# Optimization experiments

Hardware: AMD Instinct MI355X
Metric: run time of the kernel (lower is better)

## Reference

```python
import jax, jax.numpy as jnp
import numpy as np

TEMPERATURE = 8.0  # sqrt(d_k=64)


def setup_inputs() -> dict:
    key = jax.random.key(0)
    kq, kk, kv, km = jax.random.split(key, 4)
    B, S, D = 64, 2048, 64
    q = jax.random.normal(kq, (B, S, D), dtype=jnp.float32)
    k = jax.random.normal(kk, (B, S, D), dtype=jnp.float32)
    v = jax.random.normal(kv, (B, S, D), dtype=jnp.float32)
    mask = jax.random.randint(km, (B, S, S), 0, 2).astype(bool)
    return {"q": q, "k": k, "v": v, "mask": mask}


def reference(q, k, v, mask):
    # attn = q @ k^T / temperature, masked positions -> -inf
    scores = jnp.einsum("bqd,bkd->bqk", q, k) / TEMPERATURE
    scores = jnp.where(mask, -jnp.inf, scores)
    attn = jax.nn.softmax(scores, axis=-1)
    # dropout is identity in eval mode (deterministic reference)
    output = jnp.einsum("bqk,bkd->bqd", attn, v)
    return (output, attn)
```

## Files before the change

### kernel.cpp

```cpp
#include <hip/hip_runtime.h>
#include <math.h>

#define B 64
#define S 2048
#define D 64
#define INV_TEMP 0.125f

__global__ __launch_bounds__(256) void attn_scores_kernel(
    const float* __restrict__ qp, const float* __restrict__ kp,
    const int* __restrict__ maskp, float* __restrict__ attnp)
{
    __shared__ float kt[64][68];

    const int b    = blockIdx.y;
    const int wave = threadIdx.x >> 6;
    const int lane = threadIdx.x & 63;
    const int row  = blockIdx.x * 4 + wave;

    const float4* qrow = (const float4*)(qp + ((size_t)b * S + row) * D);
    float4 q4[16];
#pragma unroll
    for (int i = 0; i < 16; ++i) q4[i] = qrow[i];

    const size_t arow_base = ((size_t)b * S + row) * S;
    const float* kbase = kp + (size_t)b * S * D;

    float e[32];
    float rowsum = 0.f;

#pragma unroll
    for (int t = 0; t < 32; ++t) {
        __syncthreads();
        {
            const float4* ksrc = (const float4*)(kbase + (size_t)t * 64 * D);
#pragma unroll
            for (int i = 0; i < 4; ++i) {
                int idx = threadIdx.x + 256 * i;
                int r  = idx >> 4;
                int c4 = idx & 15;
                *((float4*)&kt[r][c4 * 4]) = ksrc[idx];
            }
        }
        __syncthreads();

        float s = 0.f;
#pragma unroll
        for (int d4 = 0; d4 < 16; ++d4) {
            float4 kv = *((const float4*)&kt[lane][d4 * 4]);
            s += q4[d4].x * kv.x + q4[d4].y * kv.y + q4[d4].z * kv.z + q4[d4].w * kv.w;
        }
        int m = maskp[arow_base + (size_t)t * 64 + lane];
        float ev = m ? 0.f : __expf(s * INV_TEMP);
        e[t] = ev;
        rowsum += ev;
    }

    float sum = rowsum;
#pragma unroll
    for (int off = 32; off > 0; off >>= 1) sum += __shfl_xor(sum, off, 64);
    float inv = 1.0f / sum;

    float* arow = attnp + arow_base;
#pragma unroll
    for (int t = 0; t < 32; ++t) arow[(size_t)t * 64 + lane] = e[t] * inv;
}

__global__ __launch_bounds__(256) void attn_pv_kernel(
    const float* __restrict__ attnp, const float* __restrict__ vp,
    float* __restrict__ outp)
{
    __shared__ float at[16][64];
    __shared__ float red[4][16][64];

    const int b  = blockIdx.y;
    const int r0 = blockIdx.x * 16;
    const int t  = threadIdx.x;
    const int d  = t & 63;
    const int g  = t >> 6;

    const float* vbase = vp + (size_t)b * S * D;
    const float* abase = attnp + ((size_t)b * S + r0) * S;

    float acc[16];
#pragma unroll
    for (int r = 0; r < 16; ++r) acc[r] = 0.f;

    for (int kt = 0; kt < 32; ++kt) {
        __syncthreads();
#pragma unroll
        for (int i = 0; i < 4; ++i) {
            int idx = t + 256 * i;
            at[idx >> 6][idx & 63] =
                abase[(size_t)(idx >> 6) * S + (size_t)kt * 64 + (idx & 63)];
        }
        __syncthreads();

#pragma unroll
        for (int kk = 0; kk < 16; ++kk) {
            int kl = g * 16 + kk;
            float vv = vbase[(size_t)(kt * 64 + kl) * D + d];
#pragma unroll
            for (int r = 0; r < 16; ++r) acc[r] += at[r][kl] * vv;
        }
    }

#pragma unroll
    for (int r = 0; r < 16; ++r) red[g][r][d] = acc[r];
    __syncthreads();
#pragma unroll
    for (int i = 0; i < 4; ++i) {
        int idx = t + 256 * i;
        int r = idx >> 6, dd = idx & 63;
        float sum = red[0][r][dd] + red[1][r][dd] + red[2][r][dd] + red[3][r][dd];
        outp[((size_t)b * S + r0 + r) * D + dd] = sum;
    }
}

extern "C" void kernel_launch(void* const* d_in, const int* in_sizes, int n_in,
                              void* d_out, int out_size, void* d_ws, size_t ws_size,
                              hipStream_t stream) {
    const float* q = (const float*)d_in[0];
    const float* k = (const float*)d_in[1];
    const float* v = (const float*)d_in[2];
    const int* mask = (const int*)d_in[3];

    float* out  = (float*)d_out;
    float* attn = out + (size_t)B * S * D;

    attn_scores_kernel<<<dim3(S / 4, B), 256, 0, stream>>>(q, k, mask, attn);
    attn_pv_kernel<<<dim3(S / 16, B), 256, 0, stream>>>(attn, v, out);
}
```

Baseline: 4.157 ms.

## Fuse QK, softmax numerator and PV into one tiled kernel with deferred normalization

Replaces the scores kernel and the PV kernel with one fused kernel. Each block handles 64 query rows, computes 4x4 register-tiled QK^T from swizzled shared memory, applies the mask and exp, writes the unnormalized probabilities, and accumulates P·V on the fly with K/V prefetched into registers. Row sums are reduced at the end to normalize the output, and a separate light kernel rescales the attention matrix in place. This avoids re-reading the full attention matrix for PV, at the cost of an extra read-modify-write pass over it for normalization.

```diff
diff --git a/kernel.cpp b/kernel.cpp
--- a/kernel.cpp
+++ b/kernel.cpp
@@ -6,113 +6,200 @@
 #define D 64
 #define INV_TEMP 0.125f
 
-__global__ __launch_bounds__(256) void attn_scores_kernel(
+__global__ __launch_bounds__(256) void attn_fused_kernel(
     const float* __restrict__ qp, const float* __restrict__ kp,
-    const int* __restrict__ maskp, float* __restrict__ attnp)
+    const float* __restrict__ vp, const int* __restrict__ maskp,
+    float* __restrict__ attnp, float* __restrict__ outp)
 {
-    __shared__ float kt[64][68];
-
+    __shared__ float qs[64][64];
+    __shared__ float ks[64][64];
+    __shared__ float vs[64][64];
+    __shared__ float es[64][64];
+
+    const int bid = blockIdx.x;
+    const int swz = (bid & 7) * 256 + (bid >> 3);
+    const int b   = swz >> 5;
+    const int r0  = (swz & 31) * 64;
+
+    const int t    = threadIdx.x;
+    const int tr   = t >> 4;
+    const int tc   = t & 15;
+    const int rr   = tr * 4;
+    const int cc   = tc * 4;
+    const int qxor = (tr & 7) << 2;
+    const int kxor = (tc & 7) << 2;
+
+    const float* kbase = kp + (size_t)b * S * D;
+    const float* vbase = vp + (size_t)b * S * D;
+
+    {
+        const float4* qsrc = (const float4*)(qp + ((size_t)b * S + r0) * D);
+#pragma unroll
+        for (int i = 0; i < 4; ++i) {
+            int idx = t + 256 * i;
+            int r = idx >> 4;
+            int c = (idx & 15) * 4;
+            *(float4*)&qs[r][c ^ (((r >> 2) & 7) << 2)] = qsrc[idx];
+        }
+    }
+
+    float4 acc[4];
+#pragma unroll
+    for (int i = 0; i < 4; ++i) acc[i] = make_float4(0.f, 0.f, 0.f, 0.f);
+    float rs[4] = {0.f, 0.f, 0.f, 0.f};
+
+    float4 kreg[4], vreg[4];
+    {
+        const float4* ksrc = (const float4*)kbase;
+        const float4* vsrc = (const float4*)vbase;
+#pragma unroll
+        for (int i = 0; i < 4; ++i) {
+            kreg[i] = ksrc[t + 256 * i];
+            vreg[i] = vsrc[t + 256 * i];
+        }
+    }
+#pragma unroll
+    for (int i = 0; i < 4; ++i) {
+        int idx = t + 256 * i;
+        int r = idx >> 4;
+        int c = (idx & 15) * 4;
+        *(float4*)&ks[r][c ^ (((r >> 2) & 7) << 2)] = kreg[i];
+        *(float4*)&vs[r][c] = vreg[i];
+    }
+    __syncthreads();
+
+#pragma unroll 1
+    for (int kt = 0; kt < 32; ++kt) {
+        if (kt < 31) {
+            const float4* ksrc = (const float4*)(kbase + (size_t)(kt + 1) * 64 * D);
+            const float4* vsrc = (const float4*)(vbase + (size_t)(kt + 1) * 64 * D);
+#pragma unroll
+            for (int i = 0; i < 4; ++i) {
+                kreg[i] = ksrc[t + 256 * i];
+                vreg[i] = vsrc[t + 256 * i];
+            }
+        }
+        int4 m4[4];
+#pragma unroll
+        for (int i = 0; i < 4; ++i) {
+            m4[i] = *(const int4*)(maskp + ((size_t)b * S + r0 + rr + i) * S
+                                   + (size_t)kt * 64 + cc);
+        }
+
+        float sc[4][4];
+#pragma unroll
+        for (int i = 0; i < 4; ++i)
+#pragma unroll
+            for (int j = 0; j < 4; ++j) sc[i][j] = 0.f;
+
+#pragma unroll
+        for (int dstep = 0; dstep < 16; ++dstep) {
+            const int dc = dstep * 4;
+            float4 q4[4], k4[4];
+#pragma unroll
+            for (int i = 0; i < 4; ++i) q4[i] = *(const float4*)&qs[rr + i][dc ^ qxor];
+#pragma unroll
+            for (int j = 0; j < 4; ++j) k4[j] = *(const float4*)&ks[cc + j][dc ^ kxor];
+#pragma unroll
+            for (int i = 0; i < 4; ++i)
+#pragma unroll
+                for (int j = 0; j < 4; ++j)
+                    sc[i][j] += q4[i].x * k4[j].x + q4[i].y * k4[j].y
+                              + q4[i].z * k4[j].z + q4[i].w * k4[j].w;
+        }
+
+        const size_t abase = ((size_t)b * S + r0 + rr) * S + (size_t)kt * 64 + cc;
+#pragma unroll
+        for (int i = 0; i < 4; ++i) {
+            float4 e4;
+            e4.x = m4[i].x ? 0.f : __expf(sc[i][0] * INV_TEMP);
+            e4.y = m4[i].y ? 0.f : __expf(sc[i][1] * INV_TEMP);
+            e4.z = m4[i].z ? 0.f : __expf(sc[i][2] * INV_TEMP);
+            e4.w = m4[i].w ? 0.f : __expf(sc[i][3] * INV_TEMP);
+            rs[i] += (e4.x + e4.y) + (e4.z + e4.w);
+            *(float4*)&es[rr + i][cc ^ qxor] = e4;
+            *(float4*)(attnp + abase + (size_t)i * S) = e4;
+        }
+        __syncthreads();
+
+#pragma unroll
+        for (int kk = 0; kk < 64; kk += 4) {
+            float4 e4[4], v4[4];
+#pragma unroll
+            for (int i = 0; i < 4; ++i) e4[i] = *(const float4*)&es[rr + i][kk ^ qxor];
+#pragma unroll
+            for (int u = 0; u < 4; ++u) v4[u] = *(const float4*)&vs[kk + u][cc];
+#pragma unroll
+            for (int i = 0; i < 4; ++i) {
+                acc[i].x += e4[i].x * v4[0].x + e4[i].y * v4[1].x
+                          + e4[i].z * v4[2].x + e4[i].w * v4[3].x;
+                acc[i].y += e4[i].x * v4[0].y + e4[i].y * v4[1].y
+                          + e4[i].z * v4[2].y + e4[i].w * v4[3].y;
+                acc[i].z += e4[i].x * v4[0].z + e4[i].y * v4[1].z
+                          + e4[i].z * v4[2].z + e4[i].w * v4[3].z;
+                acc[i].w += e4[i].x * v4[0].w + e4[i].y * v4[1].w
+                          + e4[i].z * v4[2].w + e4[i].w * v4[3].w;
+            }
+        }
+        __syncthreads();
+
+        if (kt < 31) {
+#pragma unroll
+            for (int i = 0; i < 4; ++i) {
+                int idx = t + 256 * i;
+                int r = idx >> 4;
+                int c = (idx & 15) * 4;
+                *(float4*)&ks[r][c ^ (((r >> 2) & 7) << 2)] = kreg[i];
+                *(float4*)&vs[r][c] = vreg[i];
+            }
+            __syncthreads();
+        }
+    }
+
+#pragma unroll
+    for (int i = 0; i < 4; ++i) {
+        float s = rs[i];
+        s += __shfl_xor(s, 1, 64);
+        s += __shfl_xor(s, 2, 64);
+        s += __shfl_xor(s, 4, 64);
+        s += __shfl_xor(s, 8, 64);
+        const float inv = 1.f / s;
+        float4 o;
+        o.x = acc[i].x * inv;
+        o.y = acc[i].y * inv;
+        o.z = acc[i].z * inv;
+        o.w = acc[i].w * inv;
+        *(float4*)(outp + ((size_t)b * S + r0 + rr + i) * D + cc) = o;
+    }
+}
+
+__global__ __launch_bounds__(256) void attn_norm_kernel(float* __restrict__ attnp)
+{
     const int b    = blockIdx.y;
     const int wave = threadIdx.x >> 6;
     const int lane = threadIdx.x & 63;
     const int row  = blockIdx.x * 4 + wave;
 
-    const float4* qrow = (const float4*)(qp + ((size_t)b * S + row) * D);
-    float4 q4[16];
-#pragma unroll
-    for (int i = 0; i < 16; ++i) q4[i] = qrow[i];
-
-    const size_t arow_base = ((size_t)b * S + row) * S;
-    const float* kbase = kp + (size_t)b * S * D;
-
-    float e[32];
-    float rowsum = 0.f;
-
-#pragma unroll
-    for (int t = 0; t < 32; ++t) {
-        __syncthreads();
-        {
-            const float4* ksrc = (const float4*)(kbase + (size_t)t * 64 * D);
-#pragma unroll
-            for (int i = 0; i < 4; ++i) {
-                int idx = threadIdx.x + 256 * i;
-                int r  = idx >> 4;
-                int c4 = idx & 15;
-                *((float4*)&kt[r][c4 * 4]) = ksrc[idx];
-            }
-        }
-        __syncthreads();
-
-        float s = 0.f;
-#pragma unroll
-        for (int d4 = 0; d4 < 16; ++d4) {
-            float4 kv = *((const float4*)&kt[lane][d4 * 4]);
-            s += q4[d4].x * kv.x + q4[d4].y * kv.y + q4[d4].z * kv.z + q4[d4].w * kv.w;
-        }
-        int m = maskp[arow_base + (size_t)t * 64 + lane];
-        float ev = m ? 0.f : __expf(s * INV_TEMP);
-        e[t] = ev;
-        rowsum += ev;
-    }
-
-    float sum = rowsum;
-#pragma unroll
-    for (int off = 32; off > 0; off >>= 1) sum += __shfl_xor(sum, off, 64);
-    float inv = 1.0f / sum;
-
-    float* arow = attnp + arow_base;
-#pragma unroll
-    for (int t = 0; t < 32; ++t) arow[(size_t)t * 64 + lane] = e[t] * inv;
-}
-
-__global__ __launch_bounds__(256) void attn_pv_kernel(
-    const float* __restrict__ attnp, const float* __restrict__ vp,
-    float* __restrict__ outp)
-{
-    __shared__ float at[16][64];
-    __shared__ float red[4][16][64];
-
-    const int b  = blockIdx.y;
-    const int r0 = blockIdx.x * 16;
-    const int t  = threadIdx.x;
-    const int d  = t & 63;
-    const int g  = t >> 6;
-
-    const float* vbase = vp + (size_t)b * S * D;
-    const float* abase = attnp + ((size_t)b * S + r0) * S;
-
-    float acc[16];
-#pragma unroll
-    for (int r = 0; r < 16; ++r) acc[r] = 0.f;
-
-    for (int kt = 0; kt < 32; ++kt) {
-        __syncthreads();
-#pragma unroll
-        for (int i = 0; i < 4; ++i) {
-            int idx = t + 256 * i;
-            at[idx >> 6][idx & 63] =
-                abase[(size_t)(idx >> 6) * S + (size_t)kt * 64 + (idx & 63)];
-        }
-        __syncthreads();
-
-#pragma unroll
-        for (int kk = 0; kk < 16; ++kk) {
-            int kl = g * 16 + kk;
-            float vv = vbase[(size_t)(kt * 64 + kl) * D + d];
-#pragma unroll
-            for (int r = 0; r < 16; ++r) acc[r] += at[r][kl] * vv;
-        }
-    }
-
-#pragma unroll
-    for (int r = 0; r < 16; ++r) red[g][r][d] = acc[r];
-    __syncthreads();
-#pragma unroll
-    for (int i = 0; i < 4; ++i) {
-        int idx = t + 256 * i;
-        int r = idx >> 6, dd = idx & 63;
-        float sum = red[0][r][dd] + red[1][r][dd] + red[2][r][dd] + red[3][r][dd];
-        outp[((size_t)b * S + r0 + r) * D + dd] = sum;
+    float4* arow = (float4*)(attnp + ((size_t)b * S + row) * S);
+
+    float4 x[8];
+    float s = 0.f;
+#pragma unroll
+    for (int i = 0; i < 8; ++i) {
+        x[i] = arow[lane + 64 * i];
+        s += (x[i].x + x[i].y) + (x[i].z + x[i].w);
+    }
+#pragma unroll
+    for (int off = 32; off > 0; off >>= 1) s += __shfl_xor(s, off, 64);
+    const float inv = 1.f / s;
+#pragma unroll
+    for (int i = 0; i < 8; ++i) {
+        float4 y;
+        y.x = x[i].x * inv;
+        y.y = x[i].y * inv;
+        y.z = x[i].z * inv;
+        y.w = x[i].w * inv;
+        arow[lane + 64 * i] = y;
     }
 }
 
@@ -127,6 +214,6 @@
     float* out  = (float*)d_out;
     float* attn = out + (size_t)B * S * D;
 
-    attn_scores_kernel<<<dim3(S / 4, B), 256, 0, stream>>>(q, k, mask, attn);
-    attn_pv_kernel<<<dim3(S / 16, B), 256, 0, stream>>>(attn, v, out);
+    attn_fused_kernel<<<dim3((S / 64) * B), 256, 0, stream>>>(q, k, v, mask, attn, out);
+    attn_norm_kernel<<<dim3(S / 4, B), 256, 0, stream>>>(attn);
 }
```

New measurement: 8.121 ms. 1.95x slower.
